# Kernel tuning notes

Hardware: AMD Instinct MI355X
Metric: run time of the kernel (lower is better)

Reference implementation:

```python
import jax, jax.numpy as jnp
import numpy as np

# Dims: T timesteps, B batch, C channels, HID expert hidden, E experts, K top-k
T, B, C, HID, E, K, H, W = 4, 8, 256, 1024, 8, 2, 14, 14
EPS = 1e-5       # BatchNorm eps
ALPHA = 4.0      # spikingjelly sigmoid surrogate alpha
V_TH = 1.0       # LIF threshold (spikingjelly default), v_reset = 0.0


@jax.custom_vjp
def spike_fn(u):
    # Heaviside forward, sigmoid-surrogate backward (spikingjelly surrogate.Sigmoid)
    return (u >= 0.0).astype(u.dtype)

def _spike_fwd(u):
    return (u >= 0.0).astype(u.dtype), u

def _spike_bwd(u, g):
    s = jax.nn.sigmoid(ALPHA * u)
    return (g * ALPHA * s * (1.0 - s),)

spike_fn.defvjp(_spike_fwd, _spike_bwd)


def lif(x, tau):
    """MultiStepLIFNode with hard reset (v_reset=0), detach_reset=True.
    x: (T, B, C, H, W) -> spikes of same shape."""
    def step(v, xt):
        h = v + (xt - v) / tau                      # charge
        s = spike_fn(h - V_TH)                      # fire
        v_new = h * (1.0 - jax.lax.stop_gradient(s))  # hard reset, detached spike
        return v_new, s
    _, spikes = jax.lax.scan(step, jnp.zeros_like(x[0]), x)
    return spikes


def conv1x1(x, w, b):
    # x: (T,B,Cin,H,W), w: (Cout,Cin), b: (Cout,) -- 1x1 conv == channel GEMM
    return jnp.einsum('tbchw,oc->tbohw', x, w) + b[None, None, :, None, None]


def bn(x, g, b, m, v, axis):
    # inference-mode BatchNorm with running stats, per-channel on `axis`
    shp = [1] * x.ndim
    shp[axis] = -1
    scale = g.reshape(shp) / jnp.sqrt(v.reshape(shp) + EPS)
    return (x - m.reshape(shp)) * scale + b.reshape(shp)


def expert(x, tau, w1, b1, g1, be1, m1, v1, w2, b2, g2, be2, m2, v2):
    # MS_MLP_Expert.forward: lif -> conv1x1 -> bn -> lif -> conv1x1 -> bn (no residual)
    s1 = lif(x, tau)
    h = bn(conv1x1(s1, w1, b1), g1, be1, m1, v1, axis=2)  # (T,B,HID,H,W)
    s2 = lif(h, tau)
    return bn(conv1x1(s2, w2, b2), g2, be2, m2, v2, axis=2)  # (T,B,C,H,W)


def setup_inputs() -> dict:
    key = jax.random.key(0)
    ks = jax.random.split(key, 16)
    d = {}
    d['x'] = jax.random.normal(ks[0], (T, B, C, H, W), jnp.float32)
    # router (Conv2d(C, E, 1) + BatchNorm2d(E))
    d['router_w'] = jax.random.normal(ks[1], (E, C), jnp.float32) / np.sqrt(C)
    d['router_b'] = jax.random.normal(ks[2], (E,), jnp.float32) * 0.01
    d['rbn_g'] = 1.0 + 0.1 * jax.random.normal(ks[3], (E,), jnp.float32)
    d['rbn_b'] = 0.1 * jax.random.normal(ks[4], (E,), jnp.float32)
    d['rbn_m'] = 0.1 * jax.random.normal(ks[5], (E,), jnp.float32)
    d['rbn_v'] = jax.random.uniform(ks[6], (E,), jnp.float32, 0.5, 1.5)
    # stacked expert params (leading expert axis E)
    d['fc1_w'] = jax.random.normal(ks[7], (E, HID, C), jnp.float32) / np.sqrt(C)
    d['fc1_b'] = 0.01 * jax.random.normal(ks[8], (E, HID), jnp.float32)
    d['bn1_g'] = 1.0 + 0.1 * jax.random.normal(ks[9], (E, HID), jnp.float32)
    d['bn1_b'] = 0.1 * jax.random.normal(ks[10], (E, HID), jnp.float32)
    d['bn1_m'] = 0.1 * jax.random.normal(ks[11], (E, HID), jnp.float32)
    d['bn1_v'] = jax.random.uniform(ks[12], (E, HID), jnp.float32, 0.5, 1.5)
    d['fc2_w'] = jax.random.normal(ks[13], (E, C, HID), jnp.float32) / np.sqrt(HID)
    d['fc2_b'] = 0.01 * jax.random.normal(ks[14], (E, C), jnp.float32)
    d['bn2_g'] = 1.0 + 0.1 * jax.random.normal(ks[15], (E, C), jnp.float32)
    k2 = jax.random.split(jax.random.fold_in(key, 1), 3)
    d['bn2_b'] = 0.1 * jax.random.normal(k2[0], (E, C), jnp.float32)
    d['bn2_m'] = 0.1 * jax.random.normal(k2[1], (E, C), jnp.float32)
    d['bn2_v'] = jax.random.uniform(k2[2], (E, C), jnp.float32, 0.5, 1.5)
    # expert taus: linspace(tau_min=1.5, tau_max=4.0, num_experts)
    d['taus'] = jnp.linspace(1.5, 4.0, E, dtype=jnp.float32)
    return d


def reference(x, router_w, router_b, rbn_g, rbn_b, rbn_m, rbn_v,
              fc1_w, fc1_b, bn1_g, bn1_b, bn1_m, bn1_v,
              fc2_w, fc2_b, bn2_g, bn2_b, bn2_m, bn2_v, taus):
    b_sz = x.shape[1]
    # ---- TemporalRouter ----
    xm = x.mean(axis=0)                                           # (B,C,H,W)
    r = jnp.einsum('bchw,ec->behw', xm, router_w) + router_b[None, :, None, None]
    r = bn(r, rbn_g, rbn_b, rbn_m, rbn_v, axis=1)
    logits = r.mean(axis=(-2, -1))                                # (B,E)
    probs = jax.nn.softmax(logits, axis=-1)
    topw, topi = jax.lax.top_k(probs, K)                          # (B,K)
    topw = topw / topw.sum(axis=-1, keepdims=True)
    # dense combine weights (B,E): top-k entries, 0 elsewhere; detached as in torch
    Wd = jnp.zeros((b_sz, E), x.dtype).at[jnp.arange(b_sz)[:, None], topi].add(topw)
    Wd = jax.lax.stop_gradient(Wd)
    # ---- Experts (dense dispatch: each expert over full batch, masked combine) ----
    outs = jax.vmap(expert, in_axes=(None,) + (0,) * 13)(
        x, taus, fc1_w, fc1_b, bn1_g, bn1_b, bn1_m, bn1_v,
        fc2_w, fc2_b, bn2_g, bn2_b, bn2_m, bn2_v)                 # (E,T,B,C,H,W)
    moe = jnp.einsum('etbchw,be->tbchw', outs, Wd)
    return x + moe
```

## Files before the change

kernel.cpp:

```cpp
#include <hip/hip_runtime.h>
#include <hip/hip_bf16.h>
#include <math.h>

#define T_ 4
#define B_ 8
#define C_ 256
#define HID_ 1024
#define E_ 8
#define HW_ 196
#define M_ 784
#define NPAIR_ 16
#define EPS_ 1e-5f
#define NOUT_ (T_*B_*C_*HW_)

typedef __attribute__((ext_vector_type(8))) short bf16x8;
typedef __attribute__((ext_vector_type(4))) unsigned short u16x4;
typedef __attribute__((ext_vector_type(4))) float f32x4;

__device__ inline unsigned short f2bf(float f){
  union { float f; unsigned u; } v; v.f = f;
  unsigned u = v.u;
  unsigned r = u + 0x7FFFu + ((u >> 16) & 1u);
  return (unsigned short)(r >> 16);
}
__device__ inline float bf2f(unsigned short h){
  union { unsigned u; float f; } v; v.u = ((unsigned)h) << 16;
  return v.f;
}

__device__ inline void gl16(const void* g, void* l){
  auto gp = reinterpret_cast<const unsigned int __attribute__((address_space(1)))*>(
      reinterpret_cast<uintptr_t>(g));
  auto lp = reinterpret_cast<unsigned int __attribute__((address_space(3)))*>(
      reinterpret_cast<uintptr_t>(l));
  __builtin_amdgcn_global_load_lds(gp, lp, 16, 0, 0);
}

__global__ __launch_bounds__(256) void wconv_hl_kernel(const float* __restrict__ w,
    unsigned short* __restrict__ hi, unsigned short* __restrict__ lo){
  int i = blockIdx.x * 256 + threadIdx.x;
  float4 v = ((const float4*)w)[i];
  u16x4 h, l;
  h[0]=f2bf(v.x); l[0]=f2bf(v.x - bf2f(h[0]));
  h[1]=f2bf(v.y); l[1]=f2bf(v.y - bf2f(h[1]));
  h[2]=f2bf(v.z); l[2]=f2bf(v.z - bf2f(h[2]));
  h[3]=f2bf(v.w); l[3]=f2bf(v.w - bf2f(h[3]));
  ((u16x4*)hi)[i] = h; ((u16x4*)lo)[i] = l;
}
__global__ __launch_bounds__(256) void wconv_h_kernel(const float* __restrict__ w,
    unsigned short* __restrict__ hi){
  int i = blockIdx.x * 256 + threadIdx.x;
  float4 v = ((const float4*)w)[i];
  u16x4 h;
  h[0]=f2bf(v.x); h[1]=f2bf(v.y); h[2]=f2bf(v.z); h[3]=f2bf(v.w);
  ((u16x4*)hi)[i] = h;
}

__global__ __launch_bounds__(64) void xbar_kernel(const float* __restrict__ x,
                                                  float* __restrict__ xbar){
  int bc = blockIdx.x;
  int l = threadIdx.x;
  float s = 0.f;
  for (int t = 0; t < T_; t++){
    const float* p = x + ((size_t)(t * B_ * C_) + bc) * HW_;
    for (int i = l; i < HW_; i += 64) s += p[i];
  }
  for (int off = 32; off > 0; off >>= 1) s += __shfl_down(s, off, 64);
  if (l == 0) xbar[bc] = s * (1.0f / (T_ * HW_));
}

__global__ __launch_bounds__(64) void router_kernel(const float* __restrict__ xbar,
    const float* __restrict__ rw, const float* __restrict__ rb,
    const float* __restrict__ rg, const float* __restrict__ rbb,
    const float* __restrict__ rm, const float* __restrict__ rv,
    int* __restrict__ sel_e, float* __restrict__ sel_w){
  __shared__ float lg[64];
  const int tid = threadIdx.x;
  const int b = tid >> 3, e = tid & 7;
  float dot = 0.f;
  for (int c = 0; c < C_; c++) dot += xbar[b * C_ + c] * rw[e * C_ + c];
  dot += rb[e];
  float sc = rg[e] / sqrtf(rv[e] + EPS_);
  lg[tid] = (dot - rm[e]) * sc + rbb[e];
  __syncthreads();
  if (e == 0){
    float l[E_], mx = -1e30f;
    for (int i = 0; i < E_; i++){ l[i] = lg[b * 8 + i]; mx = fmaxf(mx, l[i]); }
    float p[E_];
    for (int i = 0; i < E_; i++) p[i] = expf(l[i] - mx);
    int i1 = 0;
    for (int i = 1; i < E_; i++) if (p[i] > p[i1]) i1 = i;
    int i2 = (i1 == 0) ? 1 : 0;
    for (int i = 0; i < E_; i++) if (i != i1 && p[i] > p[i2]) i2 = i;
    float denom = p[i1] + p[i2];
    sel_e[b * 2]     = i1; sel_w[b * 2]     = p[i1] / denom;
    sel_e[b * 2 + 1] = i2; sel_w[b * 2 + 1] = p[i2] / denom;
  }
}

__global__ __launch_bounds__(256) void lif1_kernel(const float* __restrict__ x,
    const int* __restrict__ sel_e, const float* __restrict__ taus,
    unsigned short* __restrict__ s1){
  const int hw = blockIdx.x;
  const int pair = blockIdx.y;
  const int c = threadIdx.x;
  const int b = pair >> 1;
  const float tau = taus[sel_e[pair]];
  float v = 0.f;
  #pragma unroll
  for (int t = 0; t < T_; t++){
    float xv = x[((size_t)(t * B_ + b) * C_ + c) * HW_ + hw];
    float h = v + (xv - v) / tau;
    float s = (h >= 1.0f) ? 1.0f : 0.0f;
    v = h * (1.0f - s);
    s1[((size_t)pair * M_ + hw * 4 + t) * C_ + c] =
        (s > 0.5f) ? (unsigned short)0x3F80 : (unsigned short)0;
  }
}

__global__ __launch_bounds__(256) void g1_kernel(
    const unsigned short* __restrict__ s1,
    const unsigned short* __restrict__ w1h, const unsigned short* __restrict__ w1l,
    const float* __restrict__ fc1_b,
    const float* __restrict__ bn1_g, const float* __restrict__ bn1_b,
    const float* __restrict__ bn1_m, const float* __restrict__ bn1_v,
    const int* __restrict__ sel_e, const float* __restrict__ taus,
    unsigned short* __restrict__ s2)
{
  __shared__ __align__(16) unsigned short lA[2][2048];
  __shared__ __align__(16) unsigned short lBh[2][2048];
  __shared__ __align__(16) unsigned short lBl[2][2048];
  const int nt = blockIdx.x, mt = blockIdx.y, pair = blockIdx.z;
  const int e = sel_e[pair];
  const int m0 = mt * 64, n0 = nt * 64;
  const int tid = threadIdx.x, lane = tid & 63, wv = tid >> 6;
  const int l15 = lane & 15, koff = (lane >> 4) * 8;
  const int srow = wv * 16 + (lane >> 2);
  const int scol = (lane & 3) * 8;
  int arow = m0 + srow; if (arow > M_ - 1) arow = M_ - 1;
  const unsigned short* aG  = s1  + ((size_t)pair * M_ + arow) * C_ + scol;
  const unsigned short* bhG = w1h + ((size_t)e * HID_ + n0 + srow) * C_ + scol;
  const unsigned short* blG = w1l + ((size_t)e * HID_ + n0 + srow) * C_ + scol;
  const int lb = wv * 512;
  gl16(aG,  &lA[0][lb]);
  gl16(bhG, &lBh[0][lb]);
  gl16(blG, &lBl[0][lb]);
  __syncthreads();
  f32x4 acc[4] = {};
  for (int kk = 0; kk < 8; kk++){
    const int cur = kk & 1, nxt = cur ^ 1;
    if (kk < 7){
      gl16(aG  + (kk + 1) * 32, &lA[nxt][lb]);
      gl16(bhG + (kk + 1) * 32, &lBh[nxt][lb]);
      gl16(blG + (kk + 1) * 32, &lBl[nxt][lb]);
    }
    bf16x8 a = *(const bf16x8*)(&lA[cur][(wv * 16 + l15) * 32 + koff]);
    #pragma unroll
    for (int cb = 0; cb < 4; cb++){
      bf16x8 bh = *(const bf16x8*)(&lBh[cur][(cb * 16 + l15) * 32 + koff]);
      bf16x8 bl = *(const bf16x8*)(&lBl[cur][(cb * 16 + l15) * 32 + koff]);
      acc[cb] = __builtin_amdgcn_mfma_f32_16x16x32_bf16(a, bh, acc[cb], 0, 0, 0);
      acc[cb] = __builtin_amdgcn_mfma_f32_16x16x32_bf16(a, bl, acc[cb], 0, 0, 0);
    }
    __syncthreads();
  }
  const float tau = taus[e];
  const int rbase = m0 + wv * 16 + ((lane >> 4) << 2);
  if (rbase < M_){
    #pragma unroll
    for (int cb = 0; cb < 4; cb++){
      int col = n0 + cb * 16 + l15;
      int pi = e * HID_ + col;
      float sc = bn1_g[pi] / sqrtf(bn1_v[pi] + EPS_);
      float mm = bn1_m[pi], bb = bn1_b[pi], cbias = fc1_b[pi];
      float v = 0.f;
      #pragma unroll
      for (int t = 0; t < 4; t++){
        float z = acc[cb][t] + cbias;
        float hin = (z - mm) * sc + bb;
        float h = v + (hin - v) / tau;
        float s = (h >= 1.0f) ? 1.0f : 0.0f;
        v = h * (1.0f - s);
        s2[((size_t)pair * M_ + rbase + t) * HID_ + col] =
            (s > 0.5f) ? (unsigned short)0x3F80 : (unsigned short)0;
      }
    }
  }
}

__global__ __launch_bounds__(256) void g2_kernel(
    const unsigned short* __restrict__ s2,
    const unsigned short* __restrict__ w2h,
    const float* __restrict__ fc2_b,
    const float* __restrict__ bn2_g, const float* __restrict__ bn2_b,
    const float* __restrict__ bn2_m, const float* __restrict__ bn2_v,
    const int* __restrict__ sel_e, const float* __restrict__ sel_w,
    float* __restrict__ y)
{
  __shared__ __align__(16) unsigned short lA[2][2048];
  __shared__ __align__(16) unsigned short lBh[2][2048];
  const int nt = blockIdx.x, mt = blockIdx.y, pair = blockIdx.z;
  const int e = sel_e[pair];
  const float wgt = sel_w[pair];
  const int b = pair >> 1, slot = pair & 1;
  const int m0 = mt * 64, n0 = nt * 64;
  const int tid = threadIdx.x, lane = tid & 63, wv = tid >> 6;
  const int l15 = lane & 15, koff = (lane >> 4) * 8;
  const int srow = wv * 16 + (lane >> 2);
  const int scol = (lane & 3) * 8;
  int arow = m0 + srow; if (arow > M_ - 1) arow = M_ - 1;
  const unsigned short* aG  = s2  + ((size_t)pair * M_ + arow) * HID_ + scol;
  const unsigned short* bhG = w2h + ((size_t)e * C_ + n0 + srow) * HID_ + scol;
  const int lb = wv * 512;
  gl16(aG,  &lA[0][lb]);
  gl16(bhG, &lBh[0][lb]);
  __syncthreads();
  f32x4 acc[4] = {};
  for (int kk = 0; kk < 32; kk++){
    const int cur = kk & 1, nxt = cur ^ 1;
    if (kk < 31){
      gl16(aG  + (kk + 1) * 32, &lA[nxt][lb]);
      gl16(bhG + (kk + 1) * 32, &lBh[nxt][lb]);
    }
    bf16x8 a = *(const bf16x8*)(&lA[cur][(wv * 16 + l15) * 32 + koff]);
    #pragma unroll
    for (int cb = 0; cb < 4; cb++){
      bf16x8 bh = *(const bf16x8*)(&lBh[cur][(cb * 16 + l15) * 32 + koff]);
      acc[cb] = __builtin_amdgcn_mfma_f32_16x16x32_bf16(a, bh, acc[cb], 0, 0, 0);
    }
    __syncthreads();
  }
  const int rbase = m0 + wv * 16 + ((lane >> 4) << 2);
  if (rbase < M_){
    const int hw = rbase >> 2;
    #pragma unroll
    for (int cb = 0; cb < 4; cb++){
      int col = n0 + cb * 16 + l15;
      int pi = e * C_ + col;
      float sc = bn2_g[pi] / sqrtf(bn2_v[pi] + EPS_);
      float mm = bn2_m[pi], bb = bn2_b[pi], cbias = fc2_b[pi];
      #pragma unroll
      for (int t = 0; t < 4; t++){
        float z = acc[cb][t] + cbias;
        float yv = (z - mm) * sc + bb;
        y[(((size_t)slot * T_ + t) * B_ + b) * (C_ * HW_) + (size_t)col * HW_ + hw] =
            wgt * yv;
      }
    }
  }
}

__global__ __launch_bounds__(256) void combine_kernel(const float* __restrict__ x,
    const float* __restrict__ y, float* __restrict__ out){
  int i = blockIdx.x * 256 + threadIdx.x;
  float4 a  = ((const float4*)x)[i];
  float4 b0 = ((const float4*)y)[i];
  float4 b1 = ((const float4*)y)[i + NOUT_ / 4];
  float4 r;
  r.x = a.x + b0.x + b1.x;
  r.y = a.y + b0.y + b1.y;
  r.z = a.z + b0.z + b1.z;
  r.w = a.w + b0.w + b1.w;
  ((float4*)out)[i] = r;
}

extern "C" void kernel_launch(void* const* d_in, const int* in_sizes, int n_in,
                              void* d_out, int out_size, void* d_ws, size_t ws_size,
                              hipStream_t stream){
  const float* x     = (const float*)d_in[0];
  const float* rw    = (const float*)d_in[1];
  const float* rb    = (const float*)d_in[2];
  const float* rg    = (const float*)d_in[3];
  const float* rbb   = (const float*)d_in[4];
  const float* rm    = (const float*)d_in[5];
  const float* rv    = (const float*)d_in[6];
  const float* fc1_w = (const float*)d_in[7];
  const float* fc1_b = (const float*)d_in[8];
  const float* bn1_g = (const float*)d_in[9];
  const float* bn1_b = (const float*)d_in[10];
  const float* bn1_m = (const float*)d_in[11];
  const float* bn1_v = (const float*)d_in[12];
  const float* fc2_w = (const float*)d_in[13];
  const float* fc2_b = (const float*)d_in[14];
  const float* bn2_g = (const float*)d_in[15];
  const float* bn2_b = (const float*)d_in[16];
  const float* bn2_m = (const float*)d_in[17];
  const float* bn2_v = (const float*)d_in[18];
  const float* taus  = (const float*)d_in[19];
  float* out = (float*)d_out;

  char* ws = (char*)d_ws;
  size_t off = 0;
  auto alloc = [&](size_t bytes) -> char* {
    char* p = ws + off;
    off = (off + bytes + 255) & ~(size_t)255;
    return p;
  };
  const int NW = E_ * HID_ * C_;
  unsigned short* s2  = (unsigned short*)alloc((size_t)NPAIR_ * M_ * HID_ * 2);
  unsigned short* w2h = (unsigned short*)alloc((size_t)NW * 2);
  unsigned short* w1h = (unsigned short*)alloc((size_t)NW * 2);
  unsigned short* w1l = (unsigned short*)alloc((size_t)NW * 2);
  unsigned short* s1  = (unsigned short*)alloc((size_t)NPAIR_ * M_ * C_ * 2);
  float* xbar  = (float*)alloc(B_ * C_ * 4);
  int*   sel_e = (int*)alloc(NPAIR_ * 4);
  float* sel_w = (float*)alloc(NPAIR_ * 4);
  float* y = (float*)w1h;
  (void)ws_size; (void)in_sizes; (void)n_in; (void)out_size;

  wconv_hl_kernel<<<NW / 4 / 256, 256, 0, stream>>>(fc1_w, w1h, w1l);
  wconv_h_kernel <<<NW / 4 / 256, 256, 0, stream>>>(fc2_w, w2h);
  xbar_kernel<<<B_ * C_, 64, 0, stream>>>(x, xbar);
  router_kernel<<<1, 64, 0, stream>>>(xbar, rw, rb, rg, rbb, rm, rv, sel_e, sel_w);
  lif1_kernel<<<dim3(HW_, NPAIR_), 256, 0, stream>>>(x, sel_e, taus, s1);
  g1_kernel<<<dim3(HID_ / 64, (M_ + 63) / 64, NPAIR_), 256, 0, stream>>>(
      s1, w1h, w1l, fc1_b, bn1_g, bn1_b, bn1_m, bn1_v, sel_e, taus, s2);
  g2_kernel<<<dim3(C_ / 64, (M_ + 63) / 64, NPAIR_), 256, 0, stream>>>(
      s2, w2h, fc2_b, bn2_g, bn2_b, bn2_m, bn2_v, sel_e, sel_w, y);
  combine_kernel<<<NOUT_ / 4 / 256, 256, 0, stream>>>(x, y, out);
}
```

Measured before the change: 196.9 us.

## Deepen GEMM LDS pipeline to 4 stages, swizzle LDS, fuse weight conversion

Both GEMM kernels move from a double-buffered LDS scheme with two __syncthreads per step to a 4-slot ring with 3 loads in flight. Each step waits with explicit vmcnt counts, then issues one s_barrier. An XOR swizzle on the LDS column offset is applied to both the global-to-LDS store and the fragment reads, aiming to reduce bank conflicts. The two weight-conversion kernels are merged into one launch. The new scheme relies on hand-set vmcnt counts and a single barrier to protect buffer reuse, which risks races if those counts are wrong.

```diff
diff --git a/kernel.cpp b/kernel.cpp
--- a/kernel.cpp
+++ b/kernel.cpp
@@ -36,24 +36,22 @@
   __builtin_amdgcn_global_load_lds(gp, lp, 16, 0, 0);
 }
 
-__global__ __launch_bounds__(256) void wconv_hl_kernel(const float* __restrict__ w,
-    unsigned short* __restrict__ hi, unsigned short* __restrict__ lo){
+__global__ __launch_bounds__(256) void wconv_kernel(
+    const float* __restrict__ w1, const float* __restrict__ w2,
+    unsigned short* __restrict__ w1h, unsigned short* __restrict__ w1l,
+    unsigned short* __restrict__ w2h){
   int i = blockIdx.x * 256 + threadIdx.x;
-  float4 v = ((const float4*)w)[i];
+  float4 v = ((const float4*)w1)[i];
   u16x4 h, l;
   h[0]=f2bf(v.x); l[0]=f2bf(v.x - bf2f(h[0]));
   h[1]=f2bf(v.y); l[1]=f2bf(v.y - bf2f(h[1]));
   h[2]=f2bf(v.z); l[2]=f2bf(v.z - bf2f(h[2]));
   h[3]=f2bf(v.w); l[3]=f2bf(v.w - bf2f(h[3]));
-  ((u16x4*)hi)[i] = h; ((u16x4*)lo)[i] = l;
-}
-__global__ __launch_bounds__(256) void wconv_h_kernel(const float* __restrict__ w,
-    unsigned short* __restrict__ hi){
-  int i = blockIdx.x * 256 + threadIdx.x;
-  float4 v = ((const float4*)w)[i];
-  u16x4 h;
-  h[0]=f2bf(v.x); h[1]=f2bf(v.y); h[2]=f2bf(v.z); h[3]=f2bf(v.w);
-  ((u16x4*)hi)[i] = h;
+  ((u16x4*)w1h)[i] = h; ((u16x4*)w1l)[i] = l;
+  float4 u = ((const float4*)w2)[i];
+  u16x4 h2;
+  h2[0]=f2bf(u.x); h2[1]=f2bf(u.y); h2[2]=f2bf(u.z); h2[3]=f2bf(u.w);
+  ((u16x4*)w2h)[i] = h2;
 }
 
 __global__ __launch_bounds__(64) void xbar_kernel(const float* __restrict__ x,
@@ -118,6 +116,7 @@
   }
 }
 
+
 __global__ __launch_bounds__(256) void g1_kernel(
     const unsigned short* __restrict__ s1,
     const unsigned short* __restrict__ w1h, const unsigned short* __restrict__ w1l,
@@ -127,42 +126,51 @@
     const int* __restrict__ sel_e, const float* __restrict__ taus,
     unsigned short* __restrict__ s2)
 {
-  __shared__ __align__(16) unsigned short lA[2][2048];
-  __shared__ __align__(16) unsigned short lBh[2][2048];
-  __shared__ __align__(16) unsigned short lBl[2][2048];
+  __shared__ __align__(16) unsigned short lA[4][2048];
+  __shared__ __align__(16) unsigned short lBh[4][2048];
+  __shared__ __align__(16) unsigned short lBl[4][2048];
   const int nt = blockIdx.x, mt = blockIdx.y, pair = blockIdx.z;
   const int e = sel_e[pair];
   const int m0 = mt * 64, n0 = nt * 64;
   const int tid = threadIdx.x, lane = tid & 63, wv = tid >> 6;
-  const int l15 = lane & 15, koff = (lane >> 4) * 8;
+  const int l15 = lane & 15;
+  const int koffs = ((((lane >> 4) ^ (l15 & 3) ^ ((l15 >> 2) & 1)) & 3) << 3);
   const int srow = wv * 16 + (lane >> 2);
-  const int scol = (lane & 3) * 8;
+  const int scol = ((((lane & 3) ^ ((lane >> 2) & 3) ^ ((lane >> 4) & 1)) & 3) << 3);
   int arow = m0 + srow; if (arow > M_ - 1) arow = M_ - 1;
   const unsigned short* aG  = s1  + ((size_t)pair * M_ + arow) * C_ + scol;
   const unsigned short* bhG = w1h + ((size_t)e * HID_ + n0 + srow) * C_ + scol;
   const unsigned short* blG = w1l + ((size_t)e * HID_ + n0 + srow) * C_ + scol;
   const int lb = wv * 512;
-  gl16(aG,  &lA[0][lb]);
-  gl16(bhG, &lBh[0][lb]);
-  gl16(blG, &lBl[0][lb]);
-  __syncthreads();
+  #pragma unroll
+  for (int p = 0; p < 3; p++){
+    gl16(aG  + p * 32, &lA[p][lb]);
+    gl16(bhG + p * 32, &lBh[p][lb]);
+    gl16(blG + p * 32, &lBl[p][lb]);
+  }
   f32x4 acc[4] = {};
+  #pragma unroll
   for (int kk = 0; kk < 8; kk++){
-    const int cur = kk & 1, nxt = cur ^ 1;
-    if (kk < 7){
-      gl16(aG  + (kk + 1) * 32, &lA[nxt][lb]);
-      gl16(bhG + (kk + 1) * 32, &lBh[nxt][lb]);
-      gl16(blG + (kk + 1) * 32, &lBl[nxt][lb]);
-    }
-    bf16x8 a = *(const bf16x8*)(&lA[cur][(wv * 16 + l15) * 32 + koff]);
+    if (kk < 6)       asm volatile("s_waitcnt vmcnt(6)" ::: "memory");
+    else if (kk == 6) asm volatile("s_waitcnt vmcnt(3)" ::: "memory");
+    else              asm volatile("s_waitcnt vmcnt(0)" ::: "memory");
+    __builtin_amdgcn_s_barrier();
+    __builtin_amdgcn_sched_barrier(0);
+    const int cur = kk & 3;
+    bf16x8 a = *(const bf16x8*)(&lA[cur][(wv * 16 + l15) * 32 + koffs]);
     #pragma unroll
     for (int cb = 0; cb < 4; cb++){
-      bf16x8 bh = *(const bf16x8*)(&lBh[cur][(cb * 16 + l15) * 32 + koff]);
-      bf16x8 bl = *(const bf16x8*)(&lBl[cur][(cb * 16 + l15) * 32 + koff]);
+      bf16x8 bh = *(const bf16x8*)(&lBh[cur][(cb * 16 + l15) * 32 + koffs]);
+      bf16x8 bl = *(const bf16x8*)(&lBl[cur][(cb * 16 + l15) * 32 + koffs]);
       acc[cb] = __builtin_amdgcn_mfma_f32_16x16x32_bf16(a, bh, acc[cb], 0, 0, 0);
       acc[cb] = __builtin_amdgcn_mfma_f32_16x16x32_bf16(a, bl, acc[cb], 0, 0, 0);
     }
-    __syncthreads();
+    if (kk < 5){
+      const int nb = (kk + 3) & 3;
+      gl16(aG  + (kk + 3) * 32, &lA[nb][lb]);
+      gl16(bhG + (kk + 3) * 32, &lBh[nb][lb]);
+      gl16(blG + (kk + 3) * 32, &lBl[nb][lb]);
+    }
   }
   const float tau = taus[e];
   const int rbase = m0 + wv * 16 + ((lane >> 4) << 2);
@@ -197,38 +205,47 @@
     const int* __restrict__ sel_e, const float* __restrict__ sel_w,
     float* __restrict__ y)
 {
-  __shared__ __align__(16) unsigned short lA[2][2048];
-  __shared__ __align__(16) unsigned short lBh[2][2048];
+  __shared__ __align__(16) unsigned short lA[4][2048];
+  __shared__ __align__(16) unsigned short lBh[4][2048];
   const int nt = blockIdx.x, mt = blockIdx.y, pair = blockIdx.z;
   const int e = sel_e[pair];
   const float wgt = sel_w[pair];
   const int b = pair >> 1, slot = pair & 1;
   const int m0 = mt * 64, n0 = nt * 64;
   const int tid = threadIdx.x, lane = tid & 63, wv = tid >> 6;
-  const int l15 = lane & 15, koff = (lane >> 4) * 8;
+  const int l15 = lane & 15;
+  const int koffs = ((((lane >> 4) ^ (l15 & 3) ^ ((l15 >> 2) & 1)) & 3) << 3);
   const int srow = wv * 16 + (lane >> 2);
-  const int scol = (lane & 3) * 8;
+  const int scol = ((((lane & 3) ^ ((lane >> 2) & 3) ^ ((lane >> 4) & 1)) & 3) << 3);
   int arow = m0 + srow; if (arow > M_ - 1) arow = M_ - 1;
   const unsigned short* aG  = s2  + ((size_t)pair * M_ + arow) * HID_ + scol;
   const unsigned short* bhG = w2h + ((size_t)e * C_ + n0 + srow) * HID_ + scol;
   const int lb = wv * 512;
-  gl16(aG,  &lA[0][lb]);
-  gl16(bhG, &lBh[0][lb]);
-  __syncthreads();
+  #pragma unroll
+  for (int p = 0; p < 3; p++){
+    gl16(aG  + p * 32, &lA[p][lb]);
+    gl16(bhG + p * 32, &lBh[p][lb]);
+  }
   f32x4 acc[4] = {};
+  #pragma unroll
   for (int kk = 0; kk < 32; kk++){
-    const int cur = kk & 1, nxt = cur ^ 1;
-    if (kk < 31){
-      gl16(aG  + (kk + 1) * 32, &lA[nxt][lb]);
-      gl16(bhG + (kk + 1) * 32, &lBh[nxt][lb]);
-    }
-    bf16x8 a = *(const bf16x8*)(&lA[cur][(wv * 16 + l15) * 32 + koff]);
+    if (kk < 30)       asm volatile("s_waitcnt vmcnt(4)" ::: "memory");
+    else if (kk == 30) asm volatile("s_waitcnt vmcnt(2)" ::: "memory");
+    else               asm volatile("s_waitcnt vmcnt(0)" ::: "memory");
+    __builtin_amdgcn_s_barrier();
+    __builtin_amdgcn_sched_barrier(0);
+    const int cur = kk & 3;
+    bf16x8 a = *(const bf16x8*)(&lA[cur][(wv * 16 + l15) * 32 + koffs]);
     #pragma unroll
     for (int cb = 0; cb < 4; cb++){
-      bf16x8 bh = *(const bf16x8*)(&lBh[cur][(cb * 16 + l15) * 32 + koff]);
+      bf16x8 bh = *(const bf16x8*)(&lBh[cur][(cb * 16 + l15) * 32 + koffs]);
       acc[cb] = __builtin_amdgcn_mfma_f32_16x16x32_bf16(a, bh, acc[cb], 0, 0, 0);
     }
-    __syncthreads();
+    if (kk < 29){
+      const int nb = (kk + 3) & 3;
+      gl16(aG  + (kk + 3) * 32, &lA[nb][lb]);
+      gl16(bhG + (kk + 3) * 32, &lBh[nb][lb]);
+    }
   }
   const int rbase = m0 + wv * 16 + ((lane >> 4) << 2);
   if (rbase < M_){
@@ -308,8 +325,7 @@
   float* y = (float*)w1h;
   (void)ws_size; (void)in_sizes; (void)n_in; (void)out_size;
 
-  wconv_hl_kernel<<<NW / 4 / 256, 256, 0, stream>>>(fc1_w, w1h, w1l);
-  wconv_h_kernel <<<NW / 4 / 256, 256, 0, stream>>>(fc2_w, w2h);
+  wconv_kernel<<<NW / 4 / 256, 256, 0, stream>>>(fc1_w, fc2_w, w1h, w1l, w2h);
   xbar_kernel<<<B_ * C_, 64, 0, stream>>>(x, xbar);
   router_kernel<<<1, 64, 0, stream>>>(xbar, rw, rb, rg, rbb, rm, rv, sel_e, sel_w);
   lif1_kernel<<<dim3(HW_, NPAIR_), 256, 0, stream>>>(x, sel_e, taus, s1);
```

Result: no change. 197.8 us (+0.4%).
